# Kernel optimization log

Hardware: AMD Instinct MI355X
Metric: run time of the kernel (lower is better)

## Reference

```python
import jax, jax.numpy as jnp
import numpy as np

N = 50000   # nodes
E = 500000  # edges
F = 256     # node feature dim
ED = 64     # edge feature dim
H = 128     # hidden channels
O = 32      # out channels
NEG_SLOPE = 0.2
EPS = 1e-16


def setup_inputs() -> dict:
    key = jax.random.key(0)
    ks = jax.random.split(key, 16)
    s = 0.05
    return {
        "x": jax.random.normal(ks[0], (N, F), jnp.float32),
        "edge_index": jax.random.randint(ks[1], (2, E), 0, N, dtype=jnp.int32),
        "edge_attr": jax.random.normal(ks[2], (E, ED), jnp.float32),
        # layer 1 (embed): F -> H
        "W1": jax.random.normal(ks[3], (F, H), jnp.float32) * s,
        "att_src1": jax.random.normal(ks[4], (H,), jnp.float32) * s,
        "att_dst1": jax.random.normal(ks[5], (H,), jnp.float32) * s,
        "We1": jax.random.normal(ks[6], (ED, H), jnp.float32) * s,
        "att_edge1": jax.random.normal(ks[7], (H,), jnp.float32) * s,
        "b1": jnp.zeros((H,), jnp.float32),
        # layer 2 (classifier): H -> O
        "W2": jax.random.normal(ks[8], (H, O), jnp.float32) * s,
        "att_src2": jax.random.normal(ks[9], (O,), jnp.float32) * s,
        "att_dst2": jax.random.normal(ks[10], (O,), jnp.float32) * s,
        "We2": jax.random.normal(ks[11], (ED, O), jnp.float32) * s,
        "att_edge2": jax.random.normal(ks[12], (O,), jnp.float32) * s,
        "b2": jnp.zeros((O,), jnp.float32),
    }


def _add_self_loops_mean(src, dst, ea, n):
    # PyG add_self_loops(fill_value='mean'): self-loop edge_attr = mean of
    # incoming edge_attr per target node (0 for isolated nodes).
    ones = jnp.ones((ea.shape[0],), ea.dtype)
    cnt = jax.ops.segment_sum(ones, dst, num_segments=n)
    summ = jax.ops.segment_sum(ea, dst, num_segments=n)  # [n, ED]
    mean = summ / jnp.maximum(cnt, 1.0)[:, None]
    loop = jnp.arange(n, dtype=src.dtype)
    return (jnp.concatenate([src, loop]),
            jnp.concatenate([dst, loop]),
            jnp.concatenate([ea, mean], axis=0))


def _gat_conv(x, src, dst, ea, W, a_src, a_dst, We, a_edge, b):
    n = x.shape[0]
    src, dst, ea = _add_self_loops_mean(src, dst, ea, n)
    h = x @ W                       # [n, C]
    he = ea @ We                    # [E', C]
    a_s = h @ a_src                 # [n]
    a_d = h @ a_dst                 # [n]
    a_e = he @ a_edge               # [E']
    alpha = a_s[src] + a_d[dst] + a_e
    alpha = jax.nn.leaky_relu(alpha, NEG_SLOPE)
    # segment softmax over incoming edges of each target node
    m = jax.ops.segment_max(alpha, dst, num_segments=n)
    ex = jnp.exp(alpha - m[dst])
    denom = jax.ops.segment_sum(ex, dst, num_segments=n)
    coef = ex / (denom[dst] + EPS)
    out = jax.ops.segment_sum(coef[:, None] * h[src], dst, num_segments=n)
    return out + b


def reference(x, edge_index, edge_attr,
              W1, att_src1, att_dst1, We1, att_edge1, b1,
              W2, att_src2, att_dst2, We2, att_edge2, b2):
    src, dst = edge_index[0], edge_index[1]
    x1 = _gat_conv(x, src, dst, edge_attr, W1, att_src1, att_dst1, We1, att_edge1, b1)
    h = jax.nn.relu(x1)  # Dropout(0.5) is identity in eval mode
    out = _gat_conv(h, src, dst, edge_attr, W2, att_src2, att_dst2, We2, att_edge2, b2)
    return (out, h)
```

## Files before the change

kernel.cpp:

```cpp
#include <hip/hip_runtime.h>

#define N_NODES 50000
#define N_EDGES 500000
#define F_DIM 256
#define ED_DIM 64
#define H_DIM 128
#define O_DIM 32
#define NEG_SLOPE 0.2f
#define EPS_F 1e-16f

#define EB 2048

typedef __attribute__((ext_vector_type(8))) short short8;
typedef __attribute__((ext_vector_type(4))) float floatx4;

__device__ __forceinline__ unsigned short f2bf(float f) {
    union { float f; unsigned u; } c; c.f = f;
    unsigned u = c.u;
    return (unsigned short)((u + 0x7fffu + ((u >> 16) & 1u)) >> 16);
}
__device__ __forceinline__ float leaky(float a) { return a > 0.f ? a : a * NEG_SLOPE; }
__device__ __forceinline__ float dot4(float4 a, float4 b) {
    return a.x * b.x + a.y * b.y + a.z * b.z + a.w * b.w;
}

__global__ void k_prep(const float* __restrict__ We1, const float* __restrict__ aev1,
                       const float* __restrict__ We2, const float* __restrict__ aev2,
                       float* __restrict__ wv1, float* __restrict__ wv2,
                       const float* __restrict__ W1, const float* __restrict__ W2,
                       const float* __restrict__ as2v, const float* __restrict__ ad2v,
                       float* __restrict__ was2, float* __restrict__ wad2,
                       unsigned short* __restrict__ W1T, unsigned short* __restrict__ W2T,
                       int* __restrict__ cnt) {
    if (blockIdx.x == 32) {
        int t = threadIdx.x;
        if (t < 64) {
            float s = 0.f;
            for (int c = 0; c < H_DIM; c++) s += We1[t * H_DIM + c] * aev1[c];
            wv1[t] = s;
        } else if (t < 128) {
            int k = t - 64;
            float s = 0.f;
            for (int c = 0; c < O_DIM; c++) s += We2[k * O_DIM + c] * aev2[c];
            wv2[k] = s;
        } else {
            int c = t - 128;
            float s = 0.f, d = 0.f;
            for (int o = 0; o < O_DIM; o++) {
                float w = W2[c * O_DIM + o];
                s += w * as2v[o];
                d += w * ad2v[o];
            }
            was2[c] = s; wad2[c] = d;
        }
        return;
    }
    int gid = blockIdx.x * 256 + threadIdx.x;
    const int stride = 32 * 256;
    for (int i = gid; i < N_NODES; i += stride) cnt[i] = 0;
    for (int i = gid; i < H_DIM * F_DIM; i += stride) {
        int n = i >> 8, k = i & 255;
        W1T[i] = f2bf(W1[k * H_DIM + n]);
    }
    for (int i = gid; i < O_DIM * H_DIM; i += stride) {
        int n = i >> 7, k = i & 127;
        W2T[i] = f2bf(W2[k * O_DIM + n]);
    }
}

__global__ __launch_bounds__(256) void k_edge_ae(
        const float* __restrict__ ea, const int* __restrict__ dst,
        const float* __restrict__ wv1, const float* __restrict__ wv2,
        float2* __restrict__ ae12, int* __restrict__ cnt) {
    int tid = threadIdx.x;
    int wave = tid >> 6, lane = tid & 63;
    int sub = lane & 3, eg = lane >> 2;
    float4 w1[4], w2[4];
#pragma unroll
    for (int j = 0; j < 4; j++) {
        w1[j] = ((const float4*)wv1)[sub * 4 + j];
        w2[j] = ((const float4*)wv2)[sub * 4 + j];
    }
    int g0 = (blockIdx.x * 4 + wave) * 16 + eg;
    const int stride = EB * 64;
    for (int e = g0; e < N_EDGES; e += stride) {
        const float4* row = (const float4*)(ea + (size_t)e * ED_DIM + sub * 16);
        float4 q0 = row[0], q1 = row[1], q2 = row[2], q3 = row[3];
        float s1 = dot4(q0, w1[0]) + dot4(q1, w1[1]) + dot4(q2, w1[2]) + dot4(q3, w1[3]);
        float s2 = dot4(q0, w2[0]) + dot4(q1, w2[1]) + dot4(q2, w2[2]) + dot4(q3, w2[3]);
        s1 += __shfl_xor(s1, 1); s2 += __shfl_xor(s2, 1);
        s1 += __shfl_xor(s1, 2); s2 += __shfl_xor(s2, 2);
        if (sub == 0) {
            ae12[e] = make_float2(s1, s2);
            atomicAdd(&cnt[dst[e]], 1);
        }
    }
}

__global__ __launch_bounds__(256) void k_gemm1(const float* __restrict__ A,
        const unsigned short* __restrict__ BT,
        const float* __restrict__ asv, const float* __restrict__ adv,
        float* __restrict__ C, float* __restrict__ a_s, float* __restrict__ a_d, int M) {
    __shared__ unsigned short As[128 * 40];
    __shared__ unsigned short Bs[128 * 40];
    int tid = threadIdx.x;
    int wave = tid >> 6, lane = tid & 63;
    int q = lane >> 4, r = lane & 15;
    int bm0 = blockIdx.x * 128;
    floatx4 acc[2][8];
#pragma unroll
    for (int a = 0; a < 2; a++)
#pragma unroll
        for (int b = 0; b < 8; b++) acc[a][b] = (floatx4){0.f, 0.f, 0.f, 0.f};

    int rr = tid >> 3;
    int kc = tid & 7;
    for (int k0 = 0; k0 < 256; k0 += 32) {
#pragma unroll
        for (int i = 0; i < 4; i++) {
            int row = rr + 32 * i;
            int gr = bm0 + row;
            float4 v = make_float4(0.f, 0.f, 0.f, 0.f);
            if (gr < M) v = *(const float4*)(A + (size_t)gr * 256 + k0 + kc * 4);
            unsigned lo = (unsigned)f2bf(v.x) | ((unsigned)f2bf(v.y) << 16);
            unsigned hi = (unsigned)f2bf(v.z) | ((unsigned)f2bf(v.w) << 16);
            *(uint2*)&As[row * 40 + kc * 4] = make_uint2(lo, hi);
        }
#pragma unroll
        for (int i = 0; i < 2; i++) {
            int idx = tid + 256 * i;
            int n = idx >> 2, ck = idx & 3;
            *(uint4*)&Bs[n * 40 + ck * 8] = *(const uint4*)(BT + n * 256 + k0 + ck * 8);
        }
        __syncthreads();
        short8 af[2], bf[8];
#pragma unroll
        for (int rt = 0; rt < 2; rt++)
            af[rt] = *(const short8*)&As[(wave * 32 + rt * 16 + r) * 40 + q * 8];
#pragma unroll
        for (int nt = 0; nt < 8; nt++)
            bf[nt] = *(const short8*)&Bs[(nt * 16 + r) * 40 + q * 8];
#pragma unroll
        for (int rt = 0; rt < 2; rt++)
#pragma unroll
            for (int nt = 0; nt < 8; nt++)
                acc[rt][nt] = __builtin_amdgcn_mfma_f32_16x16x32_bf16(af[rt], bf[nt], acc[rt][nt], 0, 0, 0);
        __syncthreads();
    }
#pragma unroll
    for (int rt = 0; rt < 2; rt++) {
        int rowb = bm0 + wave * 32 + rt * 16 + q * 4;
        float ps[4] = {0.f, 0.f, 0.f, 0.f}, pd[4] = {0.f, 0.f, 0.f, 0.f};
#pragma unroll
        for (int nt = 0; nt < 8; nt++) {
            int col = nt * 16 + r;
            float av = asv[col], dv = adv[col];
#pragma unroll
            for (int reg = 0; reg < 4; reg++) {
                float v = acc[rt][nt][reg];
                if (rowb + reg < M) C[(size_t)(rowb + reg) * 128 + col] = v;
                ps[reg] += v * av;
                pd[reg] += v * dv;
            }
        }
#pragma unroll
        for (int reg = 0; reg < 4; reg++) {
#pragma unroll
            for (int off = 1; off < 16; off <<= 1) {
                ps[reg] += __shfl_xor(ps[reg], off);
                pd[reg] += __shfl_xor(pd[reg], off);
            }
        }
        if (r == 0) {
#pragma unroll
            for (int reg = 0; reg < 4; reg++) {
                if (rowb + reg < M) { a_s[rowb + reg] = ps[reg]; a_d[rowb + reg] = pd[reg]; }
            }
        }
    }
}

__global__ void k_scan1(const int* __restrict__ cnt, int* __restrict__ bsum, int n) {
    __shared__ int sh[256];
    int b = blockIdx.x, t = threadIdx.x;
    int base = b * 1024;
    int s = 0;
    for (int j = 0; j < 4; j++) {
        int idx = base + t * 4 + j;
        if (idx < n) s += cnt[idx];
    }
    sh[t] = s; __syncthreads();
    for (int o = 128; o > 0; o >>= 1) {
        if (t < o) sh[t] += sh[t + o];
        __syncthreads();
    }
    if (t == 0) bsum[b] = sh[0];
}

__global__ void k_scan2(const int* __restrict__ bsum, int* __restrict__ bpre,
                        int* __restrict__ offs, int nb, int n) {
    if (threadIdx.x == 0) {
        int run = 0;
        for (int b = 0; b < nb; b++) { bpre[b] = run; run += bsum[b]; }
        offs[n] = run;
    }
}

__global__ void k_scan3(const int* __restrict__ cnt, const int* __restrict__ bpre,
                        int* __restrict__ offs, int* __restrict__ cursor, int n) {
    __shared__ int sh[256];
    int b = blockIdx.x, t = threadIdx.x;
    int base = b * 1024;
    int v[4]; int s = 0;
    for (int j = 0; j < 4; j++) {
        int idx = base + t * 4 + j;
        v[j] = (idx < n) ? cnt[idx] : 0;
        s += v[j];
    }
    sh[t] = s; __syncthreads();
    for (int o = 1; o < 256; o <<= 1) {
        int x = (t >= o) ? sh[t - o] : 0;
        __syncthreads();
        sh[t] += x;
        __syncthreads();
    }
    int texcl = sh[t] - s + bpre[b];
    int run = 0;
    for (int j = 0; j < 4; j++) {
        int idx = base + t * 4 + j;
        if (idx < n) { offs[idx] = texcl + run; cursor[idx] = texcl + run; }
        run += v[j];
    }
}

__global__ __launch_bounds__(256) void k_scatter(const int* __restrict__ src, const int* __restrict__ dst,
                          const float2* __restrict__ ae12, const float* __restrict__ a_s1,
                          int* __restrict__ cursor, float4* __restrict__ csr) {
    int e = blockIdx.x * blockDim.x + threadIdx.x;
    if (e >= N_EDGES) return;
    int s = src[e];
    int d = dst[e];
    float2 a = ae12[e];
    float as = a_s1[s];
    int p = atomicAdd(&cursor[d], 1);
    csr[p] = make_float4(__int_as_float(s), a.x, a.y, as);
}

template <bool RELU>
__global__ __launch_bounds__(256) void k_agg128(const float* __restrict__ h,
                         const float* __restrict__ a_s, const float* __restrict__ a_d,
                         const int* __restrict__ offs, const float4* __restrict__ csr,
                         const float* __restrict__ bias,
                         const float* __restrict__ was2, const float* __restrict__ wad2,
                         float* __restrict__ a_s2, float* __restrict__ a_d2,
                         float* __restrict__ out) {
    int wave = threadIdx.x >> 6, lane = threadIdx.x & 63;
    int i = blockIdx.x * 4 + wave;
    int r = lane & 15;
    int g = lane >> 4;
    int rs = offs[i], re = offs[i + 1];
    int deg = re - rs;
    float adl = a_d[i];
    float4 acc0 = {0.f, 0.f, 0.f, 0.f}, acc1 = {0.f, 0.f, 0.f, 0.f};
    float dsum = 0.f, sum_ae = 0.f;
    for (int base = rs; base < re; base += 64) {
        int el = base + lane;
        float ex = 0.f, aev = 0.f; int s = 0;
        if (el < re) {
            float4 c = csr[el];
            s = __float_as_int(c.x);
            aev = c.y;
            ex = __expf(leaky(c.w + adl + aev));
        }
        dsum += ex; sum_ae += aev;
        int nv = (re - base) < 64 ? (re - base) : 64;
        int kmax = (nv + 3) >> 2;
        float ext = __shfl(ex, g);
        int st = __shfl(s, g);
        for (int k = 0; k < kmax; k++) {
            int tn = (g + 4 * (k + 1)) & 63;
            float extn = __shfl(ex, tn);
            int stn = __shfl(s, tn);
            int t = g + 4 * k;
            if (t < nv) {
                const float4* hr = (const float4*)(h + (size_t)st * 128);
                float4 v0 = hr[r * 2], v1 = hr[r * 2 + 1];
                acc0.x += ext * v0.x; acc0.y += ext * v0.y; acc0.z += ext * v0.z; acc0.w += ext * v0.w;
                acc1.x += ext * v1.x; acc1.y += ext * v1.y; acc1.z += ext * v1.z; acc1.w += ext * v1.w;
            }
            ext = extn; st = stn;
        }
    }
#pragma unroll
    for (int o = 32; o > 0; o >>= 1) {
        dsum += __shfl_xor(dsum, o);
        sum_ae += __shfl_xor(sum_ae, o);
    }
    float loop_ae = sum_ae / (float)(deg > 1 ? deg : 1);
    float al = leaky(a_s[i] + adl + loop_ae);
    float exs = __expf(al);
    float* a0 = (float*)&acc0; float* a1 = (float*)&acc1;
#pragma unroll
    for (int c = 0; c < 4; c++) {
        a0[c] += __shfl_xor(a0[c], 16); a0[c] += __shfl_xor(a0[c], 32);
        a1[c] += __shfl_xor(a1[c], 16); a1[c] += __shfl_xor(a1[c], 32);
    }
    if (g == 0) {
        float inv = 1.0f / (dsum + exs + EPS_F);
        const float4* hr = (const float4*)(h + (size_t)i * 128);
        float4 h0 = hr[r * 2], h1 = hr[r * 2 + 1];
        const float4* bp = (const float4*)bias;
        float4 b0 = bp[r * 2], b1 = bp[r * 2 + 1];
        float4 o0, o1;
        o0.x = (a0[0] + exs * h0.x) * inv + b0.x;
        o0.y = (a0[1] + exs * h0.y) * inv + b0.y;
        o0.z = (a0[2] + exs * h0.z) * inv + b0.z;
        o0.w = (a0[3] + exs * h0.w) * inv + b0.w;
        o1.x = (a1[0] + exs * h1.x) * inv + b1.x;
        o1.y = (a1[1] + exs * h1.y) * inv + b1.y;
        o1.z = (a1[2] + exs * h1.z) * inv + b1.z;
        o1.w = (a1[3] + exs * h1.w) * inv + b1.w;
        if (RELU) {
            o0.x = fmaxf(o0.x, 0.f); o0.y = fmaxf(o0.y, 0.f); o0.z = fmaxf(o0.z, 0.f); o0.w = fmaxf(o0.w, 0.f);
            o1.x = fmaxf(o1.x, 0.f); o1.y = fmaxf(o1.y, 0.f); o1.z = fmaxf(o1.z, 0.f); o1.w = fmaxf(o1.w, 0.f);
        }
        float4* op = (float4*)(out + (size_t)i * 128);
        op[r * 2] = o0;
        op[r * 2 + 1] = o1;
        float4 wsa = ((const float4*)was2)[r * 2], wsb = ((const float4*)was2)[r * 2 + 1];
        float4 wda = ((const float4*)wad2)[r * 2], wdb = ((const float4*)wad2)[r * 2 + 1];
        float ps = dot4(o0, wsa) + dot4(o1, wsb);
        float pd = dot4(o0, wda) + dot4(o1, wdb);
#pragma unroll
        for (int o = 1; o < 16; o <<= 1) {
            ps += __shfl_xor(ps, o);
            pd += __shfl_xor(pd, o);
        }
        if (r == 0) { a_s2[i] = ps; a_d2[i] = pd; }
    }
}

__global__ __launch_bounds__(256) void k_gemm2(const float* __restrict__ A,
        const unsigned short* __restrict__ BT,
        float* __restrict__ C, int M) {
    __shared__ unsigned short As[128 * 40];
    __shared__ unsigned short Bs[32 * 40];
    int tid = threadIdx.x;
    int wave = tid >> 6, lane = tid & 63;
    int q = lane >> 4, r = lane & 15;
    int bm0 = blockIdx.x * 128;
    floatx4 acc[2][2];
#pragma unroll
    for (int a = 0; a < 2; a++)
#pragma unroll
        for (int b = 0; b < 2; b++) acc[a][b] = (floatx4){0.f, 0.f, 0.f, 0.f};

    int rr = tid >> 3;
    int kc = tid & 7;
    for (int k0 = 0; k0 < 128; k0 += 32) {
#pragma unroll
        for (int i = 0; i < 4; i++) {
            int row = rr + 32 * i;
            int gr = bm0 + row;
            float4 v = make_float4(0.f, 0.f, 0.f, 0.f);
            if (gr < M) v = *(const float4*)(A + (size_t)gr * 128 + k0 + kc * 4);
            unsigned lo = (unsigned)f2bf(v.x) | ((unsigned)f2bf(v.y) << 16);
            unsigned hi = (unsigned)f2bf(v.z) | ((unsigned)f2bf(v.w) << 16);
            *(uint2*)&As[row * 40 + kc * 4] = make_uint2(lo, hi);
        }
        if (tid < 128) {
            int n = tid >> 2, ck = tid & 3;
            *(uint4*)&Bs[n * 40 + ck * 8] = *(const uint4*)(BT + n * 128 + k0 + ck * 8);
        }
        __syncthreads();
        short8 af[2], bf[2];
#pragma unroll
        for (int rt = 0; rt < 2; rt++)
            af[rt] = *(const short8*)&As[(wave * 32 + rt * 16 + r) * 40 + q * 8];
#pragma unroll
        for (int nt = 0; nt < 2; nt++)
            bf[nt] = *(const short8*)&Bs[(nt * 16 + r) * 40 + q * 8];
#pragma unroll
        for (int rt = 0; rt < 2; rt++)
#pragma unroll
            for (int nt = 0; nt < 2; nt++)
                acc[rt][nt] = __builtin_amdgcn_mfma_f32_16x16x32_bf16(af[rt], bf[nt], acc[rt][nt], 0, 0, 0);
        __syncthreads();
    }
#pragma unroll
    for (int rt = 0; rt < 2; rt++) {
        int rowb = bm0 + wave * 32 + rt * 16 + q * 4;
#pragma unroll
        for (int nt = 0; nt < 2; nt++) {
            int col = nt * 16 + r;
#pragma unroll
            for (int reg = 0; reg < 4; reg++) {
                if (rowb + reg < M) C[(size_t)(rowb + reg) * 32 + col] = acc[rt][nt][reg];
            }
        }
    }
}

__global__ __launch_bounds__(256) void k_agg32(const float* __restrict__ h,
                        const float* __restrict__ a_s, const float* __restrict__ a_d,
                        const int* __restrict__ offs, const float4* __restrict__ csr,
                        const float* __restrict__ bias,
                        float* __restrict__ out) {
    int wave = threadIdx.x >> 6, lane = threadIdx.x & 63;
    int i = blockIdx.x * 4 + wave;
    int r = lane & 7;
    int g = lane >> 3;
    int rs = offs[i], re = offs[i + 1];
    int deg = re - rs;
    float adl = a_d[i];
    float4 acc = {0.f, 0.f, 0.f, 0.f};
    float dsum = 0.f, sum_ae = 0.f;
    for (int base = rs; base < re; base += 64) {
        int el = base + lane;
        float ex = 0.f, aev = 0.f; int s = 0;
        if (el < re) {
            float4 c = csr[el];
            s = __float_as_int(c.x);
            aev = c.z;
            ex = __expf(leaky(a_s[s] + adl + aev));
        }
        dsum += ex; sum_ae += aev;
        int nv = (re - base) < 64 ? (re - base) : 64;
        int kmax = (nv + 7) >> 3;
        float ext = __shfl(ex, g);
        int st = __shfl(s, g);
        for (int k = 0; k < kmax; k++) {
            int tn = (g + 8 * (k + 1)) & 63;
            float extn = __shfl(ex, tn);
            int stn = __shfl(s, tn);
            int t = g + 8 * k;
            if (t < nv) {
                float4 v = ((const float4*)(h + (size_t)st * 32))[r];
                acc.x += ext * v.x; acc.y += ext * v.y; acc.z += ext * v.z; acc.w += ext * v.w;
            }
            ext = extn; st = stn;
        }
    }
#pragma unroll
    for (int o = 32; o > 0; o >>= 1) {
        dsum += __shfl_xor(dsum, o);
        sum_ae += __shfl_xor(sum_ae, o);
    }
    float loop_ae = sum_ae / (float)(deg > 1 ? deg : 1);
    float al = leaky(a_s[i] + adl + loop_ae);
    float exs = __expf(al);
#pragma unroll
    for (int o = 8; o < 64; o <<= 1) {
        acc.x += __shfl_xor(acc.x, o); acc.y += __shfl_xor(acc.y, o);
        acc.z += __shfl_xor(acc.z, o); acc.w += __shfl_xor(acc.w, o);
    }
    if (g == 0) {
        float inv = 1.0f / (dsum + exs + EPS_F);
        float4 hv = ((const float4*)(h + (size_t)i * 32))[r];
        float4 bv = ((const float4*)bias)[r];
        float4 ov;
        ov.x = (acc.x + exs * hv.x) * inv + bv.x;
        ov.y = (acc.y + exs * hv.y) * inv + bv.y;
        ov.z = (acc.z + exs * hv.z) * inv + bv.z;
        ov.w = (acc.w + exs * hv.w) * inv + bv.w;
        ((float4*)(out + (size_t)i * 32))[r] = ov;
    }
}

extern "C" void kernel_launch(void* const* d_in, const int* in_sizes, int n_in,
                              void* d_out, int out_size, void* d_ws, size_t ws_size,
                              hipStream_t stream) {
    const float* x    = (const float*)d_in[0];
    const int* ei     = (const int*)d_in[1];
    const float* ea   = (const float*)d_in[2];
    const float* W1   = (const float*)d_in[3];
    const float* as1v = (const float*)d_in[4];
    const float* ad1v = (const float*)d_in[5];
    const float* We1  = (const float*)d_in[6];
    const float* aev1 = (const float*)d_in[7];
    const float* b1   = (const float*)d_in[8];
    const float* W2   = (const float*)d_in[9];
    const float* as2v = (const float*)d_in[10];
    const float* ad2v = (const float*)d_in[11];
    const float* We2  = (const float*)d_in[12];
    const float* aev2 = (const float*)d_in[13];
    const float* b2   = (const float*)d_in[14];

    const int* src = ei;
    const int* dst = ei + N_EDGES;

    char* w = (char*)d_ws;
    size_t off = 0;
    auto alloc = [&](size_t bytes) -> void* {
        void* p = w + off;
        off += bytes;
        off = (off + 255) & ~(size_t)255;
        return p;
    };
    float* h1      = (float*)alloc((size_t)N_NODES * H_DIM * 4);
    float* h2      = (float*)alloc((size_t)N_NODES * O_DIM * 4);
    float2* ae12   = (float2*)alloc((size_t)N_EDGES * 8);
    int* cnt       = (int*)alloc((size_t)N_NODES * 4);
    int* offs      = (int*)alloc((size_t)(N_NODES + 1) * 4);
    int* cursor    = (int*)alloc((size_t)N_NODES * 4);
    float4* csr    = (float4*)alloc((size_t)N_EDGES * 16);
    int* bsum      = (int*)alloc(64 * 4);
    int* bpre      = (int*)alloc(64 * 4);
    float* wv1     = (float*)alloc(64 * 4);
    float* wv2     = (float*)alloc(64 * 4);
    float* was2    = (float*)alloc(128 * 4);
    float* wad2    = (float*)alloc(128 * 4);
    float* a_s1    = (float*)alloc((size_t)N_NODES * 4);
    float* a_d1    = (float*)alloc((size_t)N_NODES * 4);
    float* a_s2    = (float*)alloc((size_t)N_NODES * 4);
    float* a_d2    = (float*)alloc((size_t)N_NODES * 4);
    unsigned short* W1T = (unsigned short*)alloc((size_t)H_DIM * F_DIM * 2);
    unsigned short* W2T = (unsigned short*)alloc((size_t)O_DIM * H_DIM * 2);

    k_prep<<<33, 256, 0, stream>>>(We1, aev1, We2, aev2, wv1, wv2, W1, W2,
                                   as2v, ad2v, was2, wad2, W1T, W2T, cnt);

    k_edge_ae<<<EB, 256, 0, stream>>>(ea, dst, wv1, wv2, ae12, cnt);

    k_gemm1<<<(N_NODES + 127) / 128, 256, 0, stream>>>(x, W1T, as1v, ad1v,
                                                       h1, a_s1, a_d1, N_NODES);

    int nb = (N_NODES + 1023) / 1024;
    k_scan1<<<nb, 256, 0, stream>>>(cnt, bsum, N_NODES);
    k_scan2<<<1, 64, 0, stream>>>(bsum, bpre, offs, nb, N_NODES);
    k_scan3<<<nb, 256, 0, stream>>>(cnt, bpre, offs, cursor, N_NODES);

    k_scatter<<<(N_EDGES + 255) / 256, 256, 0, stream>>>(src, dst, ae12, a_s1,
                                                         cursor, csr);

    float* out = (float*)d_out;
    float* h_out = out + (size_t)N_NODES * O_DIM;

    k_agg128<true><<<(N_NODES + 3) / 4, 256, 0, stream>>>(h1, a_s1, a_d1, offs,
                                                          csr, b1, was2, wad2,
                                                          a_s2, a_d2, h_out);

    k_gemm2<<<(N_NODES + 127) / 128, 256, 0, stream>>>(h_out, W2T, h2, N_NODES);

    k_agg32<<<(N_NODES + 3) / 4, 256, 0, stream>>>(h2, a_s2, a_d2, offs,
                                                   csr, b2, out);
}
```

Before: 390.0 us.

## Replace three-kernel scan with single-block scan; simplify edge aggregation loops

Merges the three prefix-sum kernels into one 1024-thread single-block scan, where each thread serially sums a contiguous chunk of about 49 counts, which removes two launches and the serial block-prefix kernel. Rewrites the aggregation loops in both layers so that each lane group loads its own CSR entry and computes its own exponent directly, replacing the load-once-then-shuffle broadcast, and unrolls by two edges. This drops the shuffles and per-chunk bookkeeping but makes every lane in a group issue the same CSR load and exp, which duplicates work. The single-block scan also reads memory with a strided, uncoalesced pattern.

```diff
diff --git a/kernel.cpp b/kernel.cpp
--- a/kernel.cpp
+++ b/kernel.cpp
@@ -180,57 +180,29 @@
     }
 }
 
-__global__ void k_scan1(const int* __restrict__ cnt, int* __restrict__ bsum, int n) {
-    __shared__ int sh[256];
-    int b = blockIdx.x, t = threadIdx.x;
-    int base = b * 1024;
+__global__ __launch_bounds__(1024) void k_scan(const int* __restrict__ cnt,
+                                               int* __restrict__ offs,
+                                               int* __restrict__ cursor) {
+    __shared__ int sh[1024];
+    int t = threadIdx.x;
+    const int CHUNK = (N_NODES + 1023) / 1024;
+    int b0 = t * CHUNK;
+    int b1 = b0 + CHUNK; if (b1 > N_NODES) b1 = N_NODES;
     int s = 0;
-    for (int j = 0; j < 4; j++) {
-        int idx = base + t * 4 + j;
-        if (idx < n) s += cnt[idx];
-    }
+    for (int i = b0; i < b1; i++) s += cnt[i];
     sh[t] = s; __syncthreads();
-    for (int o = 128; o > 0; o >>= 1) {
-        if (t < o) sh[t] += sh[t + o];
-        __syncthreads();
-    }
-    if (t == 0) bsum[b] = sh[0];
-}
-
-__global__ void k_scan2(const int* __restrict__ bsum, int* __restrict__ bpre,
-                        int* __restrict__ offs, int nb, int n) {
-    if (threadIdx.x == 0) {
-        int run = 0;
-        for (int b = 0; b < nb; b++) { bpre[b] = run; run += bsum[b]; }
-        offs[n] = run;
-    }
-}
-
-__global__ void k_scan3(const int* __restrict__ cnt, const int* __restrict__ bpre,
-                        int* __restrict__ offs, int* __restrict__ cursor, int n) {
-    __shared__ int sh[256];
-    int b = blockIdx.x, t = threadIdx.x;
-    int base = b * 1024;
-    int v[4]; int s = 0;
-    for (int j = 0; j < 4; j++) {
-        int idx = base + t * 4 + j;
-        v[j] = (idx < n) ? cnt[idx] : 0;
-        s += v[j];
-    }
-    sh[t] = s; __syncthreads();
-    for (int o = 1; o < 256; o <<= 1) {
+    for (int o = 1; o < 1024; o <<= 1) {
         int x = (t >= o) ? sh[t - o] : 0;
         __syncthreads();
         sh[t] += x;
         __syncthreads();
     }
-    int texcl = sh[t] - s + bpre[b];
-    int run = 0;
-    for (int j = 0; j < 4; j++) {
-        int idx = base + t * 4 + j;
-        if (idx < n) { offs[idx] = texcl + run; cursor[idx] = texcl + run; }
-        run += v[j];
-    }
+    int run = sh[t] - s;
+    for (int i = b0; i < b1; i++) {
+        offs[i] = run; cursor[i] = run;
+        run += cnt[i];
+    }
+    if (t == 1023) offs[N_NODES] = run;
 }
 
 __global__ __launch_bounds__(256) void k_scatter(const int* __restrict__ src, const int* __restrict__ dst,
@@ -263,39 +235,33 @@
     float adl = a_d[i];
     float4 acc0 = {0.f, 0.f, 0.f, 0.f}, acc1 = {0.f, 0.f, 0.f, 0.f};
     float dsum = 0.f, sum_ae = 0.f;
-    for (int base = rs; base < re; base += 64) {
-        int el = base + lane;
-        float ex = 0.f, aev = 0.f; int s = 0;
-        if (el < re) {
-            float4 c = csr[el];
-            s = __float_as_int(c.x);
-            aev = c.y;
-            ex = __expf(leaky(c.w + adl + aev));
-        }
-        dsum += ex; sum_ae += aev;
-        int nv = (re - base) < 64 ? (re - base) : 64;
-        int kmax = (nv + 3) >> 2;
-        float ext = __shfl(ex, g);
-        int st = __shfl(s, g);
-        for (int k = 0; k < kmax; k++) {
-            int tn = (g + 4 * (k + 1)) & 63;
-            float extn = __shfl(ex, tn);
-            int stn = __shfl(s, tn);
-            int t = g + 4 * k;
-            if (t < nv) {
-                const float4* hr = (const float4*)(h + (size_t)st * 128);
-                float4 v0 = hr[r * 2], v1 = hr[r * 2 + 1];
-                acc0.x += ext * v0.x; acc0.y += ext * v0.y; acc0.z += ext * v0.z; acc0.w += ext * v0.w;
-                acc1.x += ext * v1.x; acc1.y += ext * v1.y; acc1.z += ext * v1.z; acc1.w += ext * v1.w;
-            }
-            ext = extn; st = stn;
-        }
-    }
-#pragma unroll
-    for (int o = 32; o > 0; o >>= 1) {
+
+#define P128(EL)                                                              \
+    {                                                                         \
+        float4 c = csr[EL];            \
+        int s = __float_as_int(c.x);                                          \
+        float aev = c.y;                                                      \
+        float ex = __expf(leaky(c.w + adl + aev));                            \
+        if (r == 0) { dsum += ex; sum_ae += aev; }                            \
+        const float4* hr = (const float4*)(h + (size_t)s * 128);              \
+        float4 v0 = hr[r * 2], v1 = hr[r * 2 + 1];                            \
+        acc0.x += ex * v0.x; acc0.y += ex * v0.y;                             \
+        acc0.z += ex * v0.z; acc0.w += ex * v0.w;                             \
+        acc1.x += ex * v1.x; acc1.y += ex * v1.y;                             \
+        acc1.z += ex * v1.z; acc1.w += ex * v1.w;                             \
+    }
+
+    int el = rs + g;
+    for (; el + 4 < re; el += 8) { P128(el); P128(el + 4); }
+    if (el < re) P128(el);
+#undef P128
+
+#pragma unroll
+    for (int o = 1; o < 64; o <<= 1) {
         dsum += __shfl_xor(dsum, o);
         sum_ae += __shfl_xor(sum_ae, o);
     }
+
     float loop_ae = sum_ae / (float)(deg > 1 ? deg : 1);
     float al = leaky(a_s[i] + adl + loop_ae);
     float exs = __expf(al);
@@ -415,37 +381,30 @@
     float adl = a_d[i];
     float4 acc = {0.f, 0.f, 0.f, 0.f};
     float dsum = 0.f, sum_ae = 0.f;
-    for (int base = rs; base < re; base += 64) {
-        int el = base + lane;
-        float ex = 0.f, aev = 0.f; int s = 0;
-        if (el < re) {
-            float4 c = csr[el];
-            s = __float_as_int(c.x);
-            aev = c.z;
-            ex = __expf(leaky(a_s[s] + adl + aev));
-        }
-        dsum += ex; sum_ae += aev;
-        int nv = (re - base) < 64 ? (re - base) : 64;
-        int kmax = (nv + 7) >> 3;
-        float ext = __shfl(ex, g);
-        int st = __shfl(s, g);
-        for (int k = 0; k < kmax; k++) {
-            int tn = (g + 8 * (k + 1)) & 63;
-            float extn = __shfl(ex, tn);
-            int stn = __shfl(s, tn);
-            int t = g + 8 * k;
-            if (t < nv) {
-                float4 v = ((const float4*)(h + (size_t)st * 32))[r];
-                acc.x += ext * v.x; acc.y += ext * v.y; acc.z += ext * v.z; acc.w += ext * v.w;
-            }
-            ext = extn; st = stn;
-        }
-    }
-#pragma unroll
-    for (int o = 32; o > 0; o >>= 1) {
+
+#define P32(EL)                                                               \
+    {                                                                         \
+        float4 c = csr[EL];                                                   \
+        int s = __float_as_int(c.x);                                          \
+        float aev = c.z;                                                      \
+        float ex = __expf(leaky(a_s[s] + adl + aev));                         \
+        if (r == 0) { dsum += ex; sum_ae += aev; }                            \
+        float4 v = ((const float4*)(h + (size_t)s * 32))[r];                  \
+        acc.x += ex * v.x; acc.y += ex * v.y;                                 \
+        acc.z += ex * v.z; acc.w += ex * v.w;                                 \
+    }
+
+    int el = rs + g;
+    for (; el + 8 < re; el += 16) { P32(el); P32(el + 8); }
+    if (el < re) P32(el);
+#undef P32
+
+#pragma unroll
+    for (int o = 1; o < 64; o <<= 1) {
         dsum += __shfl_xor(dsum, o);
         sum_ae += __shfl_xor(sum_ae, o);
     }
+
     float loop_ae = sum_ae / (float)(deg > 1 ? deg : 1);
     float al = leaky(a_s[i] + adl + loop_ae);
     float exs = __expf(al);
@@ -504,8 +463,6 @@
     int* offs      = (int*)alloc((size_t)(N_NODES + 1) * 4);
     int* cursor    = (int*)alloc((size_t)N_NODES * 4);
     float4* csr    = (float4*)alloc((size_t)N_EDGES * 16);
-    int* bsum      = (int*)alloc(64 * 4);
-    int* bpre      = (int*)alloc(64 * 4);
     float* wv1     = (float*)alloc(64 * 4);
     float* wv2     = (float*)alloc(64 * 4);
     float* was2    = (float*)alloc(128 * 4);
@@ -525,10 +482,7 @@
     k_gemm1<<<(N_NODES + 127) / 128, 256, 0, stream>>>(x, W1T, as1v, ad1v,
                                                        h1, a_s1, a_d1, N_NODES);
 
-    int nb = (N_NODES + 1023) / 1024;
-    k_scan1<<<nb, 256, 0, stream>>>(cnt, bsum, N_NODES);
-    k_scan2<<<1, 64, 0, stream>>>(bsum, bpre, offs, nb, N_NODES);
-    k_scan3<<<nb, 256, 0, stream>>>(cnt, bpre, offs, cursor, N_NODES);
+    k_scan<<<1, 1024, 0, stream>>>(cnt, offs, cursor);
 
     k_scatter<<<(N_EDGES + 255) / 256, 256, 0, stream>>>(src, dst, ae12, a_s1,
                                                          cursor, csr);
```

After: 487.0 us. +24.9%, slower.
